# Optimization experiments

Measured on AMD Instinct MI355X. Metric: run time of the kernel, lower is better.

The kernel has to match this reference:

```python
import jax, jax.numpy as jnp
import numpy as np
from jax import lax

DN = ('NHWC', 'HWIO', 'NHWC')

def conv2d_same(x, W, b):
    y = lax.conv_general_dilated(x, W, window_strides=(1, 1), padding='SAME', dimension_numbers=DN)
    return y + b

def maxpool2(x):
    # 2x2 max pool, stride 2, SAME padding (NHWC)
    return lax.reduce_window(x, -jnp.inf, lax.max, (1, 2, 2, 1), (1, 2, 2, 1), 'SAME')

def setup_inputs() -> dict:
    key = jax.random.key(0)
    ks = jax.random.split(key, 6)
    B, H, W, C = 8, 64, 64, 256
    s = 0.05
    return {
        'x': jax.random.normal(ks[0], (B, H, W, C), jnp.float32),
        'Wf': jax.random.normal(ks[1], (3, 3, C, C // 8), jnp.float32) * s,
        'bf': jnp.zeros((C // 8,), jnp.float32),
        'Wg': jax.random.normal(ks[2], (3, 3, C, C // 8), jnp.float32) * s,
        'bg': jnp.zeros((C // 8,), jnp.float32),
        'Wh': jax.random.normal(ks[3], (3, 3, C, C // 2), jnp.float32) * s,
        'bh': jnp.zeros((C // 2,), jnp.float32),
        'Wo': jax.random.normal(ks[4], (1, 1, C // 2, C), jnp.float32) * s,
        'bo': jnp.zeros((C,), jnp.float32),
        'gate': jnp.ones((1,), jnp.float32),
    }

def reference(x, Wf, bf, Wg, bg, Wh, bh, Wo, bo, gate):
    B, H, W, C = x.shape
    f = maxpool2(conv2d_same(x, Wf, bf))            # [B, H/2, W/2, C//8] keys
    g = conv2d_same(x, Wg, bg)                       # [B, H, W, C//8]     queries
    h = maxpool2(conv2d_same(x, Wh, bh))            # [B, H/2, W/2, C//2] values
    N, M = H * W, (H // 2) * (W // 2)
    gq = g.reshape(B, N, C // 8)
    fk = f.reshape(B, M, C // 8)
    hv = h.reshape(B, M, C // 2)
    attn = jax.nn.softmax(jnp.einsum('bnd,bmd->bnm', gq, fk), axis=-1)  # [B, N, M]
    wo = jnp.einsum('bnm,bmv->bnv', attn, hv).reshape(B, H, W, C // 2)
    out = conv2d_same(wo, Wo, bo)                    # [B, H, W, C]
    return x + gate[0] * out
```

## Files before the change

kernel.cpp:

```cpp
#include <hip/hip_runtime.h>
#include <hip/hip_fp16.h>

constexpr int B_  = 8;
constexpr int H_  = 64;
constexpr int W_  = 64;
constexpr int C_  = 256;
constexpr int CG_ = 32;
constexpr int CH_ = 128;
constexpr int NQ_ = 4096;
constexpr int NM_ = 1024;
constexpr int XP_ = 66;

typedef __attribute__((ext_vector_type(8))) _Float16 half8;
typedef __attribute__((ext_vector_type(4))) _Float16 half4;
typedef __attribute__((ext_vector_type(4))) float    f32x4;

__global__ void prep_xpad_k(const float* __restrict__ X, _Float16* __restrict__ Xpad) {
    int i8 = blockIdx.x * 256 + threadIdx.x;
    if (i8 >= B_ * XP_ * XP_ * 32) return;
    int c8 = i8 & 31;
    int px = i8 >> 5;
    int xx = px % XP_;
    int t  = px / XP_;
    int yy = t % XP_;
    int b  = t / XP_;
    half8 v;
    if (yy >= 1 && yy <= 64 && xx >= 1 && xx <= 64) {
        const float* s = X + (((size_t)(b * 64 + yy - 1) * 64) + (xx - 1)) * 256 + c8 * 8;
        float4 a = *reinterpret_cast<const float4*>(s);
        float4 bv = *reinterpret_cast<const float4*>(s + 4);
        v[0] = (_Float16)a.x;  v[1] = (_Float16)a.y;
        v[2] = (_Float16)a.z;  v[3] = (_Float16)a.w;
        v[4] = (_Float16)bv.x; v[5] = (_Float16)bv.y;
        v[6] = (_Float16)bv.z; v[7] = (_Float16)bv.w;
    } else {
        v = (half8)(_Float16)0.f;
    }
    *reinterpret_cast<half8*>(Xpad + (size_t)i8 * 8) = v;
}

__global__ void prep_wpk_k(const float* __restrict__ Wg, const float* __restrict__ Wf,
                           const float* __restrict__ Wh, _Float16* __restrict__ Wpk) {
    int i = blockIdx.x * 256 + threadIdx.x;
    if (i >= 12 * 9 * 8 * 64 * 8) return;
    int j    = i & 7;
    int lane = (i >> 3) & 63;
    int ks   = (i >> 9) & 7;
    int tap  = (i >> 12) % 9;
    int co16 = i / 36864;
    int lr = lane & 15, lk = lane >> 4;
    int co = co16 * 16 + lr;
    int kk = tap * 256 + ks * 32 + lk * 8 + j;
    float v;
    if (co < 32)      v = Wg[(size_t)kk * 32  + co];
    else if (co < 64) v = Wf[(size_t)kk * 32  + (co - 32)];
    else              v = Wh[(size_t)kk * 128 + (co - 64)];
    Wpk[i] = (_Float16)v;
}

__global__ void prep_bias_k(const float* __restrict__ bg, const float* __restrict__ bf,
                            const float* __restrict__ bh, float* __restrict__ bc) {
    int co = threadIdx.x;
    if (co >= 192) return;
    bc[co] = (co < 32) ? bg[co] : (co < 64) ? bf[co - 32] : bh[co - 64];
}

__global__ void prep_wok_k(const float* __restrict__ Wo, _Float16* __restrict__ Wok) {
    int i = blockIdx.x * 256 + threadIdx.x;
    if (i >= 16 * 4 * 64 * 8) return;
    int j    = i & 7;
    int lane = (i >> 3) & 63;
    int ks   = (i >> 9) & 3;
    int co16 = i >> 11;
    int co = co16 * 16 + (lane & 15);
    int k  = ks * 32 + (lane >> 4) * 8 + j;
    Wok[i] = (_Float16)Wo[(size_t)k * 256 + co];
}

__global__ __launch_bounds__(256, 2) void conv_mfma_k(
        const _Float16* __restrict__ Xpad, const _Float16* __restrict__ Wpk,
        const float* __restrict__ bc,
        _Float16* __restrict__ gq, float* __restrict__ fpre, float* __restrict__ hpre) {
    __shared__ char lds[XP_ * 256 * 2];
    int b   = blockIdx.x >> 6;
    int y   = blockIdx.x & 63;
    int tid = threadIdx.x;
    int wid = tid >> 6;
    int l   = tid & 63;
    int lr  = l & 15;
    int lk  = l >> 4;

    f32x4 acc[4][3];
#pragma unroll
    for (int mi = 0; mi < 4; ++mi)
#pragma unroll
        for (int nj = 0; nj < 3; ++nj) acc[mi][nj] = (f32x4)0.f;

    float4 vst[9];

#define STAGE_LOAD(KY)                                                          \
    {   const float4* sp = reinterpret_cast<const float4*>(                     \
            Xpad + ((size_t)(b * XP_ + y + (KY)) * XP_) * 256);                 \
        _Pragma("unroll")                                                       \
        for (int j = 0; j < 8; ++j) vst[j] = sp[tid + j * 256];                 \
        if (tid < 64) vst[8] = sp[tid + 2048];                                  \
    }

#define STAGE_WRITE()                                                           \
    {   _Pragma("unroll")                                                       \
        for (int j = 0; j < 8; ++j) {                                           \
            int c = tid + j * 256; int px = c >> 5;                             \
            *reinterpret_cast<float4*>(lds + ((c * 16) ^ ((px & 7) << 4))) = vst[j]; \
        }                                                                       \
        if (tid < 64) {                                                         \
            int c = tid + 2048; int px = c >> 5;                                \
            *reinterpret_cast<float4*>(lds + ((c * 16) ^ ((px & 7) << 4))) = vst[8]; \
        }                                                                       \
    }

    auto ldw = [&](int tap, int ks, half8& d0, half8& d1, half8& d2) {
        const _Float16* p = Wpk + ((((size_t)(wid * 3) * 9 + tap) * 8 + ks) * 64 + l) * 8;
        d0 = *reinterpret_cast<const half8*>(p);
        d1 = *reinterpret_cast<const half8*>(p + 36864);
        d2 = *reinterpret_cast<const half8*>(p + 73728);
    };

    STAGE_LOAD(0);
    STAGE_WRITE();
    __syncthreads();

    for (int ky = 0; ky < 3; ++ky) {
        if (ky < 2) STAGE_LOAD(ky + 1);

        int tap0 = ky * 3;
        half8 b0, b1, b2, n0, n1, n2;
        ldw(tap0, 0, b0, b1, b2);
#pragma unroll
        for (int st = 0; st < 24; ++st) {
            int kx = st >> 3, ks = st & 7;
            if (st < 23) ldw(tap0 + ((st + 1) >> 3), (st + 1) & 7, n0, n1, n2);
            half8 af[4];
#pragma unroll
            for (int mi = 0; mi < 4; ++mi) {
                int px = mi * 16 + lr + kx;
                int ad = (px * 512 + ks * 64 + lk * 16) ^ ((px & 7) << 4);
                af[mi] = *reinterpret_cast<const half8*>(lds + ad);
            }
#pragma unroll
            for (int mi = 0; mi < 4; ++mi)
                acc[mi][0] = __builtin_amdgcn_mfma_f32_16x16x32_f16(af[mi], b0, acc[mi][0], 0, 0, 0);
#pragma unroll
            for (int mi = 0; mi < 4; ++mi)
                acc[mi][1] = __builtin_amdgcn_mfma_f32_16x16x32_f16(af[mi], b1, acc[mi][1], 0, 0, 0);
#pragma unroll
            for (int mi = 0; mi < 4; ++mi)
                acc[mi][2] = __builtin_amdgcn_mfma_f32_16x16x32_f16(af[mi], b2, acc[mi][2], 0, 0, 0);
            b0 = n0; b1 = n1; b2 = n2;
        }

        if (ky < 2) {
            __syncthreads();
            STAGE_WRITE();
            __syncthreads();
        }
    }
#undef STAGE_LOAD
#undef STAGE_WRITE

    int pixbase = (b * 64 + y) * 64;
#pragma unroll
    for (int nj = 0; nj < 3; ++nj) {
        int co = wid * 48 + nj * 16 + lr;
        float bias = bc[co];
#pragma unroll
        for (int mi = 0; mi < 4; ++mi) {
#pragma unroll
            for (int r = 0; r < 4; ++r) {
                int x = mi * 16 + lk * 4 + r;
                float v = acc[mi][nj][r] + bias;
                size_t pix = pixbase + x;
                if (co < 32)        gq[pix * 32  + co]          = (_Float16)(v * 1.44269504f);
                else if (co < 64)   fpre[pix * 32  + (co - 32)] = v;
                else                hpre[pix * 128 + (co - 64)] = v;
            }
        }
    }
}

__global__ void maxpool_f16_k(const float* __restrict__ src, _Float16* __restrict__ dst) {
    int i = blockIdx.x * 256 + threadIdx.x;
    if (i >= B_ * NM_ * CG_) return;
    int c = i & 31;
    int t = i >> 5;
    int px = t & 31;
    int py = (t >> 5) & 31;
    int b  = t >> 10;
    const float* s = src + (((size_t)(b * 64 + py * 2)) * 64 + px * 2) * 32 + c;
    float v = fmaxf(fmaxf(s[0], s[32]), fmaxf(s[64 * 32], s[64 * 32 + 32]));
    dst[i] = (_Float16)v;
}

__global__ __launch_bounds__(256) void vtpool_k(const float* __restrict__ hpre,
                                                _Float16* __restrict__ Vt) {
    __shared__ float t[32][33];
    int b  = blockIdx.x >> 7;
    int kt = (blockIdx.x >> 2) & 31;
    int ct = blockIdx.x & 3;
    int tid = threadIdx.x;
#pragma unroll
    for (int i = 0; i < 4; ++i) {
        int e = tid + i * 256;
        int px = e >> 5, c = e & 31;
        const float* s = hpre + (((size_t)(b * 64 + kt * 2) * 64) + px * 2) * 128 + ct * 32 + c;
        float v = fmaxf(fmaxf(s[0], s[128]), fmaxf(s[64 * 128], s[64 * 128 + 128]));
        t[px][c] = v;
    }
    __syncthreads();
#pragma unroll
    for (int i = 0; i < 4; ++i) {
        int e = tid + i * 256;
        int c = e >> 5, px = e & 31;
        Vt[((size_t)b * 128 + ct * 32 + c) * 1024 + kt * 32 + px] = (_Float16)t[px][c];
    }
}

constexpr int PP_ = 72;

__global__ __launch_bounds__(256, 2) void attn_flash_k(
        const _Float16* __restrict__ Qf,
        const _Float16* __restrict__ Kf,
        const _Float16* __restrict__ Vt,
        _Float16* __restrict__ wo) {
    __shared__ _Float16 plds[4][16][PP_];
    __shared__ _Float16 vlds[2][8192];
    int bb  = blockIdx.x >> 6;
    int qt  = blockIdx.x & 63;
    int wid = threadIdx.x >> 6;
    int l   = threadIdx.x & 63;
    int lr  = l & 15;
    int lg  = l >> 4;
    int qbase = qt * 64 + wid * 16;

    half8 bq = *reinterpret_cast<const half8*>(
        Qf + ((size_t)bb * NQ_ + qbase + lr) * 32 + lg * 8);

    const _Float16* Kb = Kf + (size_t)bb * NM_ * 32;
    const _Float16* Vb = Vt + (size_t)bb * 128 * NM_;

    int o0  = wid * 4096 + l * 16;
    int vr0 = o0 >> 7;
    int vc  = (o0 >> 4) & 7;
    int vsw = (vr0 & 7) << 4;
    int lsw = (lr & 7) << 4;

    f32x4 acc[8];
#pragma unroll
    for (int vt = 0; vt < 8; ++vt) acc[vt] = (f32x4)0.f;
    float m_run = -1.0e30f;
    float l_lane = 0.f;

    half8 ak0, ak1, ak2, ak3;
    f32x4 s0, s1, s2, s3;
    half4 ph0, ph1, ph2, ph3;
    float4 vst[4];

#define STAGE_LOAD(T)                                                              \
    {   const _Float16* vp = Vb + (size_t)(T) * 64 + (size_t)vr0 * NM_ + vc * 8;   \
        vst[0] = *reinterpret_cast<const float4*>(vp);                             \
        vst[1] = *reinterpret_cast<const float4*>(vp + 8 * NM_);                   \
        vst[2] = *reinterpret_cast<const float4*>(vp + 16 * NM_);                  \
        vst[3] = *reinterpret_cast<const float4*>(vp + 24 * NM_);                  \
    }

#define STAGE_WRITE(BUF)                                                           \
    {   char* vbp = (char*)vlds[BUF] + (o0 ^ vsw);                                 \
        *reinterpret_cast<float4*>(vbp)        = vst[0];                           \
        *reinterpret_cast<float4*>(vbp + 1024) = vst[1];                           \
        *reinterpret_cast<float4*>(vbp + 2048) = vst[2];                           \
        *reinterpret_cast<float4*>(vbp + 3072) = vst[3];                           \
    }

#define LOADK(T)                                                                   \
    {   const _Float16* kp = Kb + (size_t)(T) * 64 * 32;                           \
        ak0 = *reinterpret_cast<const half8*>(kp + (size_t)(lr)      * 32 + lg*8); \
        ak1 = *reinterpret_cast<const half8*>(kp + (size_t)(16 + lr) * 32 + lg*8); \
        ak2 = *reinterpret_cast<const half8*>(kp + (size_t)(32 + lr) * 32 + lg*8); \
        ak3 = *reinterpret_cast<const half8*>(kp + (size_t)(48 + lr) * 32 + lg*8); \
    }

#define QK()                                                                \
    {   s0 = __builtin_amdgcn_mfma_f32_16x16x32_f16(ak0, bq, (f32x4)0.f, 0, 0, 0); \
        s1 = __builtin_amdgcn_mfma_f32_16x16x32_f16(ak1, bq, (f32x4)0.f, 0, 0, 0); \
        s2 = __builtin_amdgcn_mfma_f32_16x16x32_f16(ak2, bq, (f32x4)0.f, 0, 0, 0); \
        s3 = __builtin_amdgcn_mfma_f32_16x16x32_f16(ak3, bq, (f32x4)0.f, 0, 0, 0); \
    }

#define SOFTMAX()                                                           \
    {   float lm = fmaxf(fmaxf(fmaxf(s0[0], s0[1]), fmaxf(s0[2], s0[3])),   \
                         fmaxf(fmaxf(s1[0], s1[1]), fmaxf(s1[2], s1[3])));  \
        lm = fmaxf(lm, fmaxf(fmaxf(fmaxf(s2[0], s2[1]), fmaxf(s2[2], s2[3])), \
                             fmaxf(fmaxf(s3[0], s3[1]), fmaxf(s3[2], s3[3])))); \
        if (__any(lm > m_run + 11.0f)) {                                    \
            float mx = lm;                                                  \
            mx = fmaxf(mx, __shfl_xor(mx, 16, 64));                         \
            mx = fmaxf(mx, __shfl_xor(mx, 32, 64));                         \
            float mnew  = fmaxf(m_run, mx);                                 \
            float alpha = exp2f(m_run - mnew);                              \
            l_lane *= alpha;                                                \
            _Pragma("unroll")                                               \
            for (int r = 0; r < 4; ++r) {                                   \
                float ar = __shfl(alpha, 4 * lg + r, 64);                   \
                _Pragma("unroll")                                           \
                for (int vt = 0; vt < 8; ++vt) acc[vt][r] *= ar;            \
            }                                                               \
            m_run = mnew;                                                   \
        }                                                                   \
        float ps = 0.f;                                                     \
        {   float p0 = exp2f(s0[0]-m_run), p1 = exp2f(s0[1]-m_run);         \
            float p2 = exp2f(s0[2]-m_run), p3 = exp2f(s0[3]-m_run);         \
            ps += (p0+p1)+(p2+p3);                                          \
            ph0[0]=(_Float16)p0; ph0[1]=(_Float16)p1;                       \
            ph0[2]=(_Float16)p2; ph0[3]=(_Float16)p3; }                     \
        {   float p0 = exp2f(s1[0]-m_run), p1 = exp2f(s1[1]-m_run);         \
            float p2 = exp2f(s1[2]-m_run), p3 = exp2f(s1[3]-m_run);         \
            ps += (p0+p1)+(p2+p3);                                          \
            ph1[0]=(_Float16)p0; ph1[1]=(_Float16)p1;                       \
            ph1[2]=(_Float16)p2; ph1[3]=(_Float16)p3; }                     \
        {   float p0 = exp2f(s2[0]-m_run), p1 = exp2f(s2[1]-m_run);         \
            float p2 = exp2f(s2[2]-m_run), p3 = exp2f(s2[3]-m_run);         \
            ps += (p0+p1)+(p2+p3);                                          \
            ph2[0]=(_Float16)p0; ph2[1]=(_Float16)p1;                       \
            ph2[2]=(_Float16)p2; ph2[3]=(_Float16)p3; }                     \
        {   float p0 = exp2f(s3[0]-m_run), p1 = exp2f(s3[1]-m_run);         \
            float p2 = exp2f(s3[2]-m_run), p3 = exp2f(s3[3]-m_run);         \
            ps += (p0+p1)+(p2+p3);                                          \
            ph3[0]=(_Float16)p0; ph3[1]=(_Float16)p1;                       \
            ph3[2]=(_Float16)p2; ph3[3]=(_Float16)p3; }                     \
        l_lane += ps;                                                       \
    }

#define WRITEP()                                                            \
    {   *reinterpret_cast<half4*>(&plds[wid][lr][ 0 + 4*lg]) = ph0;         \
        *reinterpret_cast<half4*>(&plds[wid][lr][16 + 4*lg]) = ph1;         \
        *reinterpret_cast<half4*>(&plds[wid][lr][32 + 4*lg]) = ph2;         \
        *reinterpret_cast<half4*>(&plds[wid][lr][48 + 4*lg]) = ph3;         \
    }

#define PV(BUF)                                                             \
    {   half8 ap0 = *reinterpret_cast<const half8*>(&plds[wid][lr][8*lg]);  \
        half8 ap1 = *reinterpret_cast<const half8*>(&plds[wid][lr][32 + 8*lg]); \
        const char* vbp = (const char*)vlds[BUF];                           \
        _Pragma("unroll")                                                   \
        for (int vt = 0; vt < 8; ++vt) {                                    \
            int ra = (vt * 16 + lr) * 128;                                  \
            half8 bv = *reinterpret_cast<const half8*>(                     \
                vbp + ((ra + lg * 16) ^ lsw));                              \
            acc[vt] = __builtin_amdgcn_mfma_f32_16x16x32_f16(ap0, bv, acc[vt], 0, 0, 0); \
        }                                                                   \
        _Pragma("unroll")                                                   \
        for (int vt = 0; vt < 8; ++vt) {                                    \
            int ra = (vt * 16 + lr) * 128;                                  \
            half8 bv = *reinterpret_cast<const half8*>(                     \
                vbp + ((ra + (4 + lg) * 16) ^ lsw));                        \
            acc[vt] = __builtin_amdgcn_mfma_f32_16x16x32_f16(ap1, bv, acc[vt], 0, 0, 0); \
        }                                                                   \
    }

    STAGE_LOAD(0);
    STAGE_WRITE(0);
    LOADK(0);
    __syncthreads();
    QK(); SOFTMAX();

    for (int t = 0; t < 16; ++t) {
        if (t < 15) { STAGE_LOAD(t + 1); LOADK(t + 1); }
        WRITEP();
        PV(t & 1);
        if (t < 15) STAGE_WRITE((t + 1) & 1);
        __syncthreads();
        if (t < 15) { QK(); SOFTMAX(); }
    }

#undef STAGE_LOAD
#undef STAGE_WRITE
#undef LOADK
#undef QK
#undef SOFTMAX
#undef WRITEP
#undef PV

    float lsum = l_lane;
    lsum += __shfl_xor(lsum, 16, 64);
    lsum += __shfl_xor(lsum, 32, 64);
    float inv = 1.f / lsum;
#pragma unroll
    for (int r = 0; r < 4; ++r) {
        float ir = __shfl(inv, 4 * lg + r, 64);
        _Float16* orow = wo + ((size_t)bb * NQ_ + qbase + 4 * lg + r) * 128 + lr;
#pragma unroll
        for (int vt = 0; vt < 8; ++vt) orow[vt * 16] = (_Float16)(acc[vt][r] * ir);
    }
}

__global__ __launch_bounds__(256, 2) void conv1x1_mfma_k(
        const _Float16* __restrict__ wo, const _Float16* __restrict__ Wok,
        const float* __restrict__ bo, const float* __restrict__ X,
        const float* __restrict__ gate, float* __restrict__ out) {
    __shared__ char lds[64 * 256];
    int pix0 = blockIdx.x * 64;
    int tid = threadIdx.x;
    int wq = tid >> 6;
    int l  = tid & 63;
    int lr = l & 15;
    int lg = l >> 4;

    {
        const float4* sp = reinterpret_cast<const float4*>(wo + (size_t)pix0 * 128);
#pragma unroll
        for (int j = 0; j < 4; ++j) {
            int c = tid + j * 256;
            int px = c >> 4;
            *reinterpret_cast<float4*>(lds + ((c * 16) ^ ((px & 7) << 4))) = sp[c];
        }
    }
    __syncthreads();

    f32x4 acc[4][4];
#pragma unroll
    for (int mi = 0; mi < 4; ++mi)
#pragma unroll
        for (int nj = 0; nj < 4; ++nj) acc[mi][nj] = (f32x4)0.f;

#pragma unroll
    for (int ks = 0; ks < 4; ++ks) {
        half8 ap[4];
#pragma unroll
        for (int mi = 0; mi < 4; ++mi) {
            int px = mi * 16 + lr;
            int ad = (px * 256 + ks * 64 + lg * 16) ^ ((px & 7) << 4);
            ap[mi] = *reinterpret_cast<const half8*>(lds + ad);
        }
#pragma unroll
        for (int nj = 0; nj < 4; ++nj) {
            int co16 = wq * 4 + nj;
            half8 bv = *reinterpret_cast<const half8*>(
                Wok + (((size_t)co16 * 4 + ks) * 64 + l) * 8);
#pragma unroll
            for (int mi = 0; mi < 4; ++mi)
                acc[mi][nj] = __builtin_amdgcn_mfma_f32_16x16x32_f16(ap[mi], bv, acc[mi][nj], 0, 0, 0);
        }
    }

    float gt = gate[0];
#pragma unroll
    for (int nj = 0; nj < 4; ++nj) {
        int co = wq * 64 + nj * 16 + lr;
        float bias = bo[co];
#pragma unroll
        for (int mi = 0; mi < 4; ++mi) {
#pragma unroll
            for (int r = 0; r < 4; ++r) {
                size_t o = (size_t)(pix0 + mi * 16 + lg * 4 + r) * 256 + co;
                out[o] = X[o] + gt * (acc[mi][nj][r] + bias);
            }
        }
    }
}

extern "C" void kernel_launch(void* const* d_in, const int* in_sizes, int n_in,
                              void* d_out, int out_size, void* d_ws, size_t ws_size,
                              hipStream_t stream) {
    const float* X    = (const float*)d_in[0];
    const float* Wf   = (const float*)d_in[1];
    const float* bf   = (const float*)d_in[2];
    const float* Wg   = (const float*)d_in[3];
    const float* bg   = (const float*)d_in[4];
    const float* Wh   = (const float*)d_in[5];
    const float* bh   = (const float*)d_in[6];
    const float* Wo   = (const float*)d_in[7];
    const float* bo   = (const float*)d_in[8];
    const float* gate = (const float*)d_in[9];
    float* out = (float*)d_out;

    float* ws   = (float*)d_ws;
    float* fpre = ws;
    float* hpre = fpre + 1048576;
    _Float16* gq = (_Float16*)(hpre + 4194304);
    _Float16* Kf = (_Float16*)((float*)gq + 524288);
    _Float16* Vt = (_Float16*)((float*)Kf + 131072);
    _Float16* Xpad = (_Float16*)((float*)Vt + 524288);
    _Float16* Wpk  = (_Float16*)((float*)Xpad + 4460544);
    float* bc   = (float*)Wpk + 221184;
    _Float16* Wok = (_Float16*)(bc + 192);
    _Float16* wobuf = (_Float16*)hpre;

    prep_xpad_k<<<(B_ * XP_ * XP_ * 32 + 255) / 256, 256, 0, stream>>>(X, Xpad);
    prep_wpk_k<<<(12 * 9 * 8 * 64 * 8 + 255) / 256, 256, 0, stream>>>(Wg, Wf, Wh, Wpk);
    prep_bias_k<<<1, 256, 0, stream>>>(bg, bf, bh, bc);
    prep_wok_k<<<(16 * 4 * 64 * 8 + 255) / 256, 256, 0, stream>>>(Wo, Wok);
    conv_mfma_k<<<B_ * H_, 256, 0, stream>>>(Xpad, Wpk, bc, gq, fpre, hpre);
    maxpool_f16_k<<<(B_ * NM_ * CG_ + 255) / 256, 256, 0, stream>>>(fpre, Kf);
    vtpool_k<<<B_ * 32 * 4, 256, 0, stream>>>(hpre, Vt);
    attn_flash_k<<<B_ * 64, 256, 0, stream>>>(gq, Kf, Vt, wobuf);
    conv1x1_mfma_k<<<(B_ * NQ_) / 64, 256, 0, stream>>>(wobuf, Wok, bo, X, gate, out);
}
```

Before: 123.1 us.

## Split 3x3 conv over kernel rows into separate blocks with fp16 partial sums

The fused conv kernel now launches three times as many blocks, each handling one kernel row (ky) and writing fp16 partial outputs to per-ky buffers. The consumers (maxpool, vtpool, attention Q load) sum the three partials. The goal is more parallelism across the CUs (512 blocks was low occupancy) and removing the serialized LDS restaging between kernel rows. In exchange it triples partial-output traffic, adds a reduction step in the downstream kernels, and sums fp16 partials, which costs some precision.

Result: faster. 113.6 us (-7.7%).

```diff
diff --git a/kernel.cpp b/kernel.cpp
--- a/kernel.cpp
+++ b/kernel.cpp
@@ -10,6 +10,9 @@
 constexpr int NQ_ = 4096;
 constexpr int NM_ = 1024;
 constexpr int XP_ = 66;
+
+constexpr int GP_ = 1048576;
+constexpr int HP_ = 4194304;
 
 typedef __attribute__((ext_vector_type(8))) _Float16 half8;
 typedef __attribute__((ext_vector_type(4))) _Float16 half4;
@@ -77,46 +80,49 @@
     Wok[i] = (_Float16)Wo[(size_t)k * 256 + co];
 }
 
-__global__ __launch_bounds__(256, 2) void conv_mfma_k(
+__global__ __launch_bounds__(256, 4) void conv_mfma_k(
         const _Float16* __restrict__ Xpad, const _Float16* __restrict__ Wpk,
         const float* __restrict__ bc,
-        _Float16* __restrict__ gq, float* __restrict__ fpre, float* __restrict__ hpre) {
+        _Float16* __restrict__ gpart, _Float16* __restrict__ fpart,
+        _Float16* __restrict__ hpart) {
     __shared__ char lds[XP_ * 256 * 2];
-    int b   = blockIdx.x >> 6;
-    int y   = blockIdx.x & 63;
+    int bid = blockIdx.x;
+    int lg  = (bid & 7) * 192 + (bid >> 3);
+    int ky  = lg % 3;
+    int iy  = lg / 3;
+    int b   = iy >> 6;
+    int y   = iy & 63;
     int tid = threadIdx.x;
     int wid = tid >> 6;
     int l   = tid & 63;
     int lr  = l & 15;
     int lk  = l >> 4;
 
+    {
+        const float4* sp = reinterpret_cast<const float4*>(
+            Xpad + ((size_t)(b * XP_ + y + ky) * XP_) * 256);
+        float4 vst[8];
+#pragma unroll
+        for (int j = 0; j < 8; ++j) vst[j] = sp[tid + j * 256];
+        float4 tl;
+        if (tid < 64) tl = sp[tid + 2048];
+#pragma unroll
+        for (int j = 0; j < 8; ++j) {
+            int c = tid + j * 256; int px = c >> 5;
+            *reinterpret_cast<float4*>(lds + ((c * 16) ^ ((px & 7) << 4))) = vst[j];
+        }
+        if (tid < 64) {
+            int c = tid + 2048; int px = c >> 5;
+            *reinterpret_cast<float4*>(lds + ((c * 16) ^ ((px & 7) << 4))) = tl;
+        }
+    }
+    __syncthreads();
+
     f32x4 acc[4][3];
 #pragma unroll
     for (int mi = 0; mi < 4; ++mi)
 #pragma unroll
         for (int nj = 0; nj < 3; ++nj) acc[mi][nj] = (f32x4)0.f;
-
-    float4 vst[9];
-
-#define STAGE_LOAD(KY)                                                          \
-    {   const float4* sp = reinterpret_cast<const float4*>(                     \
-            Xpad + ((size_t)(b * XP_ + y + (KY)) * XP_) * 256);                 \
-        _Pragma("unroll")                                                       \
-        for (int j = 0; j < 8; ++j) vst[j] = sp[tid + j * 256];                 \
-        if (tid < 64) vst[8] = sp[tid + 2048];                                  \
-    }
-
-#define STAGE_WRITE()                                                           \
-    {   _Pragma("unroll")                                                       \
-        for (int j = 0; j < 8; ++j) {                                           \
-            int c = tid + j * 256; int px = c >> 5;                             \
-            *reinterpret_cast<float4*>(lds + ((c * 16) ^ ((px & 7) << 4))) = vst[j]; \
-        }                                                                       \
-        if (tid < 64) {                                                         \
-            int c = tid + 2048; int px = c >> 5;                                \
-            *reinterpret_cast<float4*>(lds + ((c * 16) ^ ((px & 7) << 4))) = vst[8]; \
-        }                                                                       \
-    }
 
     auto ldw = [&](int tap, int ks, half8& d0, half8& d1, half8& d2) {
         const _Float16* p = Wpk + ((((size_t)(wid * 3) * 9 + tap) * 8 + ks) * 64 + l) * 8;
@@ -125,53 +131,38 @@
         d2 = *reinterpret_cast<const half8*>(p + 73728);
     };
 
-    STAGE_LOAD(0);
-    STAGE_WRITE();
-    __syncthreads();
-
-    for (int ky = 0; ky < 3; ++ky) {
-        if (ky < 2) STAGE_LOAD(ky + 1);
-
-        int tap0 = ky * 3;
-        half8 b0, b1, b2, n0, n1, n2;
-        ldw(tap0, 0, b0, b1, b2);
-#pragma unroll
-        for (int st = 0; st < 24; ++st) {
-            int kx = st >> 3, ks = st & 7;
-            if (st < 23) ldw(tap0 + ((st + 1) >> 3), (st + 1) & 7, n0, n1, n2);
-            half8 af[4];
-#pragma unroll
-            for (int mi = 0; mi < 4; ++mi) {
-                int px = mi * 16 + lr + kx;
-                int ad = (px * 512 + ks * 64 + lk * 16) ^ ((px & 7) << 4);
-                af[mi] = *reinterpret_cast<const half8*>(lds + ad);
-            }
-#pragma unroll
-            for (int mi = 0; mi < 4; ++mi)
-                acc[mi][0] = __builtin_amdgcn_mfma_f32_16x16x32_f16(af[mi], b0, acc[mi][0], 0, 0, 0);
-#pragma unroll
-            for (int mi = 0; mi < 4; ++mi)
-                acc[mi][1] = __builtin_amdgcn_mfma_f32_16x16x32_f16(af[mi], b1, acc[mi][1], 0, 0, 0);
-#pragma unroll
-            for (int mi = 0; mi < 4; ++mi)
-                acc[mi][2] = __builtin_amdgcn_mfma_f32_16x16x32_f16(af[mi], b2, acc[mi][2], 0, 0, 0);
-            b0 = n0; b1 = n1; b2 = n2;
-        }
-
-        if (ky < 2) {
-            __syncthreads();
-            STAGE_WRITE();
-            __syncthreads();
-        }
-    }
-#undef STAGE_LOAD
-#undef STAGE_WRITE
+    int tap0 = ky * 3;
+    half8 b0, b1, b2, n0, n1, n2;
+    ldw(tap0, 0, b0, b1, b2);
+#pragma unroll
+    for (int st = 0; st < 24; ++st) {
+        int kx = st >> 3, ks = st & 7;
+        if (st < 23) ldw(tap0 + ((st + 1) >> 3), (st + 1) & 7, n0, n1, n2);
+        half8 af[4];
+#pragma unroll
+        for (int mi = 0; mi < 4; ++mi) {
+            int px = mi * 16 + lr + kx;
+            int ad = (px * 512 + ks * 64 + lk * 16) ^ ((px & 7) << 4);
+            af[mi] = *reinterpret_cast<const half8*>(lds + ad);
+        }
+#pragma unroll
+        for (int mi = 0; mi < 4; ++mi)
+            acc[mi][0] = __builtin_amdgcn_mfma_f32_16x16x32_f16(af[mi], b0, acc[mi][0], 0, 0, 0);
+#pragma unroll
+        for (int mi = 0; mi < 4; ++mi)
+            acc[mi][1] = __builtin_amdgcn_mfma_f32_16x16x32_f16(af[mi], b1, acc[mi][1], 0, 0, 0);
+#pragma unroll
+        for (int mi = 0; mi < 4; ++mi)
+            acc[mi][2] = __builtin_amdgcn_mfma_f32_16x16x32_f16(af[mi], b2, acc[mi][2], 0, 0, 0);
+        b0 = n0; b1 = n1; b2 = n2;
+    }
 
     int pixbase = (b * 64 + y) * 64;
+    bool addb = (ky == 1);
 #pragma unroll
     for (int nj = 0; nj < 3; ++nj) {
         int co = wid * 48 + nj * 16 + lr;
-        float bias = bc[co];
+        float bias = addb ? bc[co] : 0.f;
 #pragma unroll
         for (int mi = 0; mi < 4; ++mi) {
 #pragma unroll
@@ -179,15 +170,18 @@
                 int x = mi * 16 + lk * 4 + r;
                 float v = acc[mi][nj][r] + bias;
                 size_t pix = pixbase + x;
-                if (co < 32)        gq[pix * 32  + co]          = (_Float16)(v * 1.44269504f);
-                else if (co < 64)   fpre[pix * 32  + (co - 32)] = v;
-                else                hpre[pix * 128 + (co - 64)] = v;
+                if (co < 32)
+                    gpart[(size_t)ky * GP_ + pix * 32 + co] = (_Float16)(v * 1.44269504f);
+                else if (co < 64)
+                    fpart[(size_t)ky * GP_ + pix * 32 + (co - 32)] = (_Float16)v;
+                else
+                    hpart[(size_t)ky * HP_ + pix * 128 + (co - 64)] = (_Float16)v;
             }
         }
     }
 }
 
-__global__ void maxpool_f16_k(const float* __restrict__ src, _Float16* __restrict__ dst) {
+__global__ void maxpool_f16_k(const _Float16* __restrict__ fp, _Float16* __restrict__ dst) {
     int i = blockIdx.x * 256 + threadIdx.x;
     if (i >= B_ * NM_ * CG_) return;
     int c = i & 31;
@@ -195,24 +189,32 @@
     int px = t & 31;
     int py = (t >> 5) & 31;
     int b  = t >> 10;
-    const float* s = src + (((size_t)(b * 64 + py * 2)) * 64 + px * 2) * 32 + c;
-    float v = fmaxf(fmaxf(s[0], s[32]), fmaxf(s[64 * 32], s[64 * 32 + 32]));
+    size_t base = (((size_t)(b * 64 + py * 2)) * 64 + px * 2) * 32 + c;
+    const _Float16* p1 = fp + GP_;
+    const _Float16* p2 = fp + 2 * GP_;
+    auto val = [&](size_t o) { return (float)fp[o] + (float)p1[o] + (float)p2[o]; };
+    float v = fmaxf(fmaxf(val(base), val(base + 32)),
+                    fmaxf(val(base + 64 * 32), val(base + 64 * 32 + 32)));
     dst[i] = (_Float16)v;
 }
 
-__global__ __launch_bounds__(256) void vtpool_k(const float* __restrict__ hpre,
+__global__ __launch_bounds__(256) void vtpool_k(const _Float16* __restrict__ hp,
                                                 _Float16* __restrict__ Vt) {
     __shared__ float t[32][33];
     int b  = blockIdx.x >> 7;
     int kt = (blockIdx.x >> 2) & 31;
     int ct = blockIdx.x & 3;
     int tid = threadIdx.x;
+    const _Float16* p1 = hp + HP_;
+    const _Float16* p2 = hp + 2 * (size_t)HP_;
 #pragma unroll
     for (int i = 0; i < 4; ++i) {
         int e = tid + i * 256;
         int px = e >> 5, c = e & 31;
-        const float* s = hpre + (((size_t)(b * 64 + kt * 2) * 64) + px * 2) * 128 + ct * 32 + c;
-        float v = fmaxf(fmaxf(s[0], s[128]), fmaxf(s[64 * 128], s[64 * 128 + 128]));
+        size_t base = (((size_t)(b * 64 + kt * 2) * 64) + px * 2) * 128 + ct * 32 + c;
+        auto val = [&](size_t o) { return (float)hp[o] + (float)p1[o] + (float)p2[o]; };
+        float v = fmaxf(fmaxf(val(base), val(base + 128)),
+                        fmaxf(val(base + 64 * 128), val(base + 64 * 128 + 128)));
         t[px][c] = v;
     }
     __syncthreads();
@@ -227,7 +229,7 @@
 constexpr int PP_ = 72;
 
 __global__ __launch_bounds__(256, 2) void attn_flash_k(
-        const _Float16* __restrict__ Qf,
+        const _Float16* __restrict__ Qp,
         const _Float16* __restrict__ Kf,
         const _Float16* __restrict__ Vt,
         _Float16* __restrict__ wo) {
@@ -241,8 +243,10 @@
     int lg  = l >> 4;
     int qbase = qt * 64 + wid * 16;
 
-    half8 bq = *reinterpret_cast<const half8*>(
-        Qf + ((size_t)bb * NQ_ + qbase + lr) * 32 + lg * 8);
+    const _Float16* gp = Qp + ((size_t)bb * NQ_ + qbase + lr) * 32 + lg * 8;
+    half8 bq = *reinterpret_cast<const half8*>(gp);
+    bq = bq + *reinterpret_cast<const half8*>(gp + GP_);
+    bq = bq + *reinterpret_cast<const half8*>(gp + 2 * GP_);
 
     const _Float16* Kb = Kf + (size_t)bb * NM_ * 32;
     const _Float16* Vb = Vt + (size_t)bb * 128 * NM_;
@@ -482,25 +486,24 @@
     const float* gate = (const float*)d_in[9];
     float* out = (float*)d_out;
 
-    float* ws   = (float*)d_ws;
-    float* fpre = ws;
-    float* hpre = fpre + 1048576;
-    _Float16* gq = (_Float16*)(hpre + 4194304);
-    _Float16* Kf = (_Float16*)((float*)gq + 524288);
-    _Float16* Vt = (_Float16*)((float*)Kf + 131072);
-    _Float16* Xpad = (_Float16*)((float*)Vt + 524288);
-    _Float16* Wpk  = (_Float16*)((float*)Xpad + 4460544);
-    float* bc   = (float*)Wpk + 221184;
-    _Float16* Wok = (_Float16*)(bc + 192);
-    _Float16* wobuf = (_Float16*)hpre;
+    _Float16* gpart = (_Float16*)d_ws;
+    _Float16* fpart = gpart + 3 * (size_t)GP_;
+    _Float16* hpart = fpart + 3 * (size_t)GP_;
+    _Float16* Kf    = hpart + 3 * (size_t)HP_;
+    _Float16* Vt    = Kf + 262144;
+    _Float16* Xpad  = Vt + 1048576;
+    _Float16* Wpk   = Xpad + 8921088;
+    float*    bc    = (float*)(Wpk + 442368);
+    _Float16* Wok   = (_Float16*)(bc + 192);
+    _Float16* wobuf = hpart;
 
     prep_xpad_k<<<(B_ * XP_ * XP_ * 32 + 255) / 256, 256, 0, stream>>>(X, Xpad);
     prep_wpk_k<<<(12 * 9 * 8 * 64 * 8 + 255) / 256, 256, 0, stream>>>(Wg, Wf, Wh, Wpk);
     prep_bias_k<<<1, 256, 0, stream>>>(bg, bf, bh, bc);
     prep_wok_k<<<(16 * 4 * 64 * 8 + 255) / 256, 256, 0, stream>>>(Wo, Wok);
-    conv_mfma_k<<<B_ * H_, 256, 0, stream>>>(Xpad, Wpk, bc, gq, fpre, hpre);
-    maxpool_f16_k<<<(B_ * NM_ * CG_ + 255) / 256, 256, 0, stream>>>(fpre, Kf);
-    vtpool_k<<<B_ * 32 * 4, 256, 0, stream>>>(hpre, Vt);
-    attn_flash_k<<<B_ * 64, 256, 0, stream>>>(gq, Kf, Vt, wobuf);
+    conv_mfma_k<<<3 * B_ * H_, 256, 0, stream>>>(Xpad, Wpk, bc, gpart, fpart, hpart);
+    maxpool_f16_k<<<(B_ * NM_ * CG_ + 255) / 256, 256, 0, stream>>>(fpart, Kf);
+    vtpool_k<<<B_ * 32 * 4, 256, 0, stream>>>(hpart, Vt);
+    attn_flash_k<<<B_ * 64, 256, 0, stream>>>(gpart, Kf, Vt, wobuf);
     conv1x1_mfma_k<<<(B_ * NQ_) / 64, 256, 0, stream>>>(wobuf, Wok, bo, X, gate, out);
 }
```
